# Kernel tuning notes

Hardware: AMD Instinct MI355X
Metric: run time of the kernel (lower is better)

## Reference

```python
import jax, jax.numpy as jnp
import numpy as np

BEAM = 4
START = 1


def setup_inputs() -> dict:
    key = jax.random.key(0)
    ks = jax.random.split(key, 10)
    S, B, H, E, V = 32, 16, 1024, 256, 32000
    Din = E + E + H  # embed + enc_input_step + enc_output_step
    sc = 0.02
    return {
        "enc_h_n": jax.random.normal(ks[0], (1, B, H), jnp.float32),
        "enc_c_n": jax.random.normal(ks[1], (1, B, H), jnp.float32),
        "enc_outputs": jax.random.normal(ks[2], (S, B, H), jnp.float32),
        "enc_inputs": jax.random.normal(ks[3], (S, B, E), jnp.float32),
        "embed": jax.random.normal(ks[4], (V, E), jnp.float32) * sc,
        "w_ih": jax.random.normal(ks[5], (Din, 4 * H), jnp.float32) * sc,
        "w_hh": jax.random.normal(ks[6], (H, 4 * H), jnp.float32) * sc,
        "b_lstm": jnp.zeros((4 * H,), jnp.float32),
        "w_out": jax.random.normal(ks[7], (H, V), jnp.float32) * sc,
        "b_out": jnp.zeros((V,), jnp.float32),
    }


def reference(enc_h_n, enc_c_n, enc_outputs, enc_inputs,
              embed, w_ih, w_hh, b_lstm, w_out, b_out):
    S, B, _ = enc_inputs.shape
    H = enc_h_n.shape[2]
    V = w_out.shape[1]
    K = BEAM

    def decode(word, h, c, ein, eout):
        # word: [B] int, h/c: [B,H], ein: [B,E], eout: [B,H]
        x = jnp.concatenate([embed[word], ein, eout], axis=-1)  # [B,Din]
        gates = x @ w_ih + h @ w_hh + b_lstm                    # [B,4H]
        i, f, g, o = jnp.split(gates, 4, axis=-1)
        c2 = jax.nn.sigmoid(f) * c + jax.nn.sigmoid(i) * jnp.tanh(g)
        h2 = jax.nn.sigmoid(o) * jnp.tanh(c2)
        logits = h2 @ w_out + b_out                             # [B,V]
        return logits, h2, c2

    # ---- init_beam_search (step 0) ----
    h0, c0 = enc_h_n[0], enc_c_n[0]
    word0 = jnp.full((B,), START, dtype=jnp.int32)
    logits0, h1, c1 = decode(word0, h0, c0, enc_inputs[0], enc_outputs[0])
    probs0 = jax.nn.softmax(logits0, axis=-1)
    top_v, top_i = jax.lax.top_k(probs0, K)  # [B,K]
    # NOTE: original code never updates current_scores inside the loop -> constant
    scores = top_v

    h = jnp.broadcast_to(h1, (K, B, H)) + 0.0  # per-beam hidden state copies
    c = jnp.broadcast_to(c1, (K, B, H)) + 0.0
    word = top_i  # [B,K]

    decode_beams = jax.vmap(decode, in_axes=(1, 0, 0, None, None))

    def step(carry, xs):
        h, c, word = carry
        ein, eout = xs
        logits, h2, c2 = decode_beams(word, h, c, ein, eout)  # [K,B,V]
        probs = jax.nn.softmax(logits, axis=-1)
        # space_search layout: beam b occupies cols [b*V, (b+1)*V); tile repeats
        # each beam score V times -> equivalent to broadcast over vocab axis.
        space = jnp.transpose(probs, (1, 0, 2)) * scores[:, :, None]  # [B,K,V]
        _, ti = jax.lax.top_k(space.reshape(B, K * V), K)             # [B,K]
        word2 = ti % V
        return (h2, c2, word2), ti

    (_, _, _), tis = jax.lax.scan(step, (h, c, word),
                                  (enc_inputs[1:], enc_outputs[1:]))
    out = jnp.concatenate([top_i[None], tis], axis=0)  # [S,B,K]
    return jnp.transpose(out, (2, 1, 0)).astype(jnp.int32)  # [K,B,S]
```

## Files before the change

kernel.cpp:

```cpp
#include <hip/hip_runtime.h>
#include <math.h>

#define S_LEN 32
#define B_N   16
#define H_N   1024
#define E_N   256
#define V_N   32000
#define KBEAM 4
#define DIN   1536
#define D2    2560
#define R_N   64
#define NDS   20
#define NB    500

typedef _Float16 f16;
typedef f16   f16x8 __attribute__((ext_vector_type(8)));
typedef float f32x4 __attribute__((ext_vector_type(4)));
#define MFMA(A,B,C) __builtin_amdgcn_mfma_f32_16x16x32_f16(A,B,C,0,0,0)

__device__ __forceinline__ float sigmf(float x){ return 1.0f/(1.0f+expf(-x)); }
__device__ __forceinline__ bool better(float v1,int i1,float v2,int i2){
  return (v1>v2) || (v1==v2 && i1<i2);
}
__device__ __forceinline__ void ins4(float bv,int bi,
    float&av0,float&av1,float&av2,float&av3,int&ai0,int&ai1,int&ai2,int&ai3){
  if (better(bv,bi,av3,ai3)){ av3=bv; ai3=bi;
    if (better(av3,ai3,av2,ai2)){ float t=av2;av2=av3;av3=t; int q=ai2;ai2=ai3;ai3=q;
      if (better(av2,ai2,av1,ai1)){ t=av1;av1=av2;av2=t; q=ai1;ai1=ai2;ai2=q;
        if (better(av1,ai1,av0,ai0)){ t=av0;av0=av1;av1=t; q=ai0;ai0=ai1;ai1=q; } } } }
}

#define FMA16(w4, h4) { \
  acc[0][0]=fmaf(w4.x,h4.x,acc[0][0]); acc[0][1]=fmaf(w4.x,h4.y,acc[0][1]); \
  acc[0][2]=fmaf(w4.x,h4.z,acc[0][2]); acc[0][3]=fmaf(w4.x,h4.w,acc[0][3]); \
  acc[1][0]=fmaf(w4.y,h4.x,acc[1][0]); acc[1][1]=fmaf(w4.y,h4.y,acc[1][1]); \
  acc[1][2]=fmaf(w4.y,h4.z,acc[1][2]); acc[1][3]=fmaf(w4.y,h4.w,acc[1][3]); \
  acc[2][0]=fmaf(w4.z,h4.x,acc[2][0]); acc[2][1]=fmaf(w4.z,h4.y,acc[2][1]); \
  acc[2][2]=fmaf(w4.z,h4.z,acc[2][2]); acc[2][3]=fmaf(w4.z,h4.w,acc[2][3]); \
  acc[3][0]=fmaf(w4.w,h4.x,acc[3][0]); acc[3][1]=fmaf(w4.w,h4.y,acc[3][1]); \
  acc[3][2]=fmaf(w4.w,h4.z,acc[3][2]); acc[3][3]=fmaf(w4.w,h4.w,acc[3][3]); }

__global__ __launch_bounds__(256) void k_init(
    const float* __restrict__ enc_h_n, const float* __restrict__ enc_c_n,
    const float* __restrict__ enc_outputs, const float* __restrict__ enc_inputs,
    const float* __restrict__ embed, float* __restrict__ x, float* __restrict__ c){
  int r = blockIdx.x, tid = threadIdx.x, b = r & 15;
  float* xr = x + (size_t)r*D2;
  xr[tid]        = embed[E_N + tid];
  xr[E_N + tid]  = enc_inputs[b*E_N + tid];
  #pragma unroll
  for (int q=0;q<4;++q) xr[2*E_N + q*256 + tid] = enc_outputs[b*H_N + q*256 + tid];
  #pragma unroll
  for (int q=0;q<4;++q) xr[DIN + q*256 + tid]   = enc_h_n[b*H_N + q*256 + tid];
  #pragma unroll
  for (int q=0;q<4;++q) c[(size_t)r*H_N + q*256 + tid] = enc_c_n[b*H_N + q*256 + tid];
}

__global__ __launch_bounds__(256) void k_convw(
    const float* __restrict__ w, f16* __restrict__ wpk){
  __shared__ f16 Th[64][66];
  __shared__ f16 Tl[64][66];
  int v0 = blockIdx.x*64, d0 = blockIdx.y*64;
  int tid = threadIdx.x;
  int r = tid >> 4, cq = (tid & 15)*4;
  #pragma unroll
  for (int rr=0; rr<4; ++rr){
    int d = r + rr*16;
    float4 x = *(const float4*)&w[(size_t)(d0+d)*V_N + v0 + cq];
    f16 h;
    h=(f16)x.x; Th[d][cq+0]=h; Tl[d][cq+0]=(f16)((x.x-(float)h)*4096.0f);
    h=(f16)x.y; Th[d][cq+1]=h; Tl[d][cq+1]=(f16)((x.y-(float)h)*4096.0f);
    h=(f16)x.z; Th[d][cq+2]=h; Tl[d][cq+2]=(f16)((x.z-(float)h)*4096.0f);
    h=(f16)x.w; Th[d][cq+3]=h; Tl[d][cq+3]=(f16)((x.w-(float)h)*4096.0f);
  }
  __syncthreads();
  int T2 = tid >> 6, l = tid & 63;
  int lm = l & 15, kq = l >> 4;
  int Tg = blockIdx.x*4 + T2;
  #pragma unroll
  for (int ks2=0; ks2<2; ++ks2){
    int ksg = blockIdx.y*2 + ks2;
    f16x8 a, b2;
    #pragma unroll
    for (int i=0;i<8;++i){
      int dd = ks2*32 + kq*8 + i;
      a[i]  = Th[dd][T2*16 + lm];
      b2[i] = Tl[dd][T2*16 + lm];
    }
    size_t base = ((size_t)(Tg*32 + ksg)*2)*512 + l*8;
    *(f16x8*)&wpk[base]       = a;
    *(f16x8*)&wpk[base + 512] = b2;
  }
}

#define GWLD(d, off) (*(const float4*)((((d) < DIN) ? (w_ih + (size_t)(d)*4096) \
                       : (w_hh + (size_t)((d)-DIN)*4096)) + (off)))
__global__ __launch_bounds__(256) void k_gates(
    const float* __restrict__ x, const float* __restrict__ w_ih,
    const float* __restrict__ w_hh, float* __restrict__ gpart){
  int tid = threadIdx.x;
  int jt = blockIdx.x, ks = blockIdx.y;
  int cx = tid & 15, ry = tid >> 4;
  int cb = jt*64;
  int wdd = tid >> 4, wseg = tid & 15;
  int xrow = tid >> 3, xseg = tid & 7;

  __shared__ float Wt0[32][64], Wt1[32][64];
  __shared__ float Xt0[32][68], Xt1[32][68];

  float acc[4][4];
  #pragma unroll
  for (int cc=0;cc<4;++cc)
    #pragma unroll
    for (int rr=0;rr<4;++rr) acc[cc][rr]=0.f;

  int d0 = ks*128;
  const float* xp0 = x + (size_t)xrow*D2 + d0 + xseg*4;
  const float* xp1 = x + (size_t)(xrow+32)*D2 + d0 + xseg*4;

#define GLQ(WA,WB,X0,X1, ch) { int d_ = d0 + (ch)*32; \
  WA = GWLD(d_+wdd,    cb+wseg*4); \
  WB = GWLD(d_+16+wdd, cb+wseg*4); \
  X0 = *(const float4*)(xp0 + (ch)*32); \
  X1 = *(const float4*)(xp1 + (ch)*32); }
#define GSQ(Wt,Xt, WA,WB,X0,X1) { \
  *(float4*)&Wt[wdd][wseg*4]    = WA; \
  *(float4*)&Wt[wdd+16][wseg*4] = WB; \
  Xt[xseg*4+0][xrow] = X0.x; Xt[xseg*4+1][xrow] = X0.y; \
  Xt[xseg*4+2][xrow] = X0.z; Xt[xseg*4+3][xrow] = X0.w; \
  Xt[xseg*4+0][xrow+32] = X1.x; Xt[xseg*4+1][xrow+32] = X1.y; \
  Xt[xseg*4+2][xrow+32] = X1.z; Xt[xseg*4+3][xrow+32] = X1.w; }
#define GCQ(Wt,Xt) { _Pragma("unroll 8") for (int dd=0; dd<32; ++dd){ \
    float4 w4 = *(const float4*)&Wt[dd][cx*4]; \
    float4 h4 = *(const float4*)&Xt[dd][ry*4]; \
    FMA16(w4, h4) } }

  float4 wA0,wB0,x00,x10, wA1,wB1,x01,x11;
  GLQ(wA0,wB0,x00,x10, 0)
  GSQ(Wt0,Xt0, wA0,wB0,x00,x10)
  GLQ(wA1,wB1,x01,x11, 1)
  __syncthreads();

  for (int ch=0; ch<4; ch+=2){
    if (ch+2<4) GLQ(wA0,wB0,x00,x10, ch+2)
    GSQ(Wt1,Xt1, wA1,wB1,x01,x11)
    GCQ(Wt0,Xt0)
    __syncthreads();
    if (ch+3<4) GLQ(wA1,wB1,x01,x11, ch+3)
    if (ch+2<4) GSQ(Wt0,Xt0, wA0,wB0,x00,x10)
    GCQ(Wt1,Xt1)
    if (ch+2<4) __syncthreads();
  }
  #pragma unroll
  for (int rr=0;rr<4;++rr){
    float4 o; o.x=acc[0][rr]; o.y=acc[1][rr]; o.z=acc[2][rr]; o.w=acc[3][rr];
    *(float4*)&gpart[((size_t)(ks*R_N + ry*4+rr))*4096 + cb + cx*4] = o;
  }
}

__global__ __launch_bounds__(256) void k_lstm(
    const float* __restrict__ gpart, const float* __restrict__ b_lstm,
    float* __restrict__ c, float* __restrict__ xn, float* __restrict__ h2t,
    f16* __restrict__ hpk){
  int r = blockIdx.x, tid = threadIdx.x;
  int j = blockIdx.y*256 + tid;
  float gi = b_lstm[j], gf = b_lstm[1024+j], gg = b_lstm[2048+j], go = b_lstm[3072+j];
  #pragma unroll
  for (int ds=0; ds<NDS; ++ds){
    size_t base = ((size_t)ds*R_N + r)*4096;
    gi += gpart[base + j];      gf += gpart[base + 1024 + j];
    gg += gpart[base + 2048+j]; go += gpart[base + 3072 + j];
  }
  float cv = c[(size_t)r*H_N + j];
  float c2 = sigmf(gf)*cv + sigmf(gi)*tanhf(gg);
  float h2 = sigmf(go)*tanhf(c2);
  c[(size_t)r*H_N + j] = c2;
  xn[(size_t)r*D2 + DIN + j] = h2;
  h2t[(size_t)j*R_N + r] = h2;
  f16 hh = (f16)h2;
  int m = r >> 4, lm = r & 15;
  int ks = j >> 5, kq = (j & 31) >> 3, i = j & 7;
  int l = lm + 16*kq;
  size_t base2 = ((size_t)(m*32 + ks)*2)*512 + l*8 + i;
  hpk[base2]       = hh;
  hpk[base2 + 512] = (f16)((h2 - (float)hh)*4096.0f);
}

__global__ __launch_bounds__(256) void k_logits_mfma(
    const f16* __restrict__ wpk, const f16* __restrict__ hpk,
    const float* __restrict__ b_out,
    float* __restrict__ pm, float* __restrict__ pz,
    float* __restrict__ pv, int* __restrict__ pi){
  int tid = threadIdx.x;
  int lane = tid & 63;
  int wv = tid >> 6;
  int T  = blockIdx.x*4 + wv;
  int vb = T*16;

  const f16* wp  = wpk + ((size_t)(T*32))*2*512 + lane*8;
  const f16* hp0 = hpk + ((size_t)(0*32))*2*512 + lane*8;
  const f16* hp1 = hpk + ((size_t)(1*32))*2*512 + lane*8;
  const f16* hp2 = hpk + ((size_t)(2*32))*2*512 + lane*8;
  const f16* hp3 = hpk + ((size_t)(3*32))*2*512 + lane*8;

  f32x4 c10={0,0,0,0}, c11={0,0,0,0}, c12={0,0,0,0}, c13={0,0,0,0};
  f32x4 c20={0,0,0,0}, c21={0,0,0,0}, c22={0,0,0,0}, c23={0,0,0,0};

  f16x8 Bh0,Bl0,A0h0,A1h0,A2h0,A3h0,A0l0,A1l0,A2l0,A3l0;
  f16x8 Bh1,Bl1,A0h1,A1h1,A2h1,A3h1,A0l1,A1l1,A2l1,A3l1;

#define LOADSET(S, s) { size_t o_ = (size_t)(s)*1024; \
  Bh##S  = *(const f16x8*)(wp + o_);  Bl##S  = *(const f16x8*)(wp + o_ + 512); \
  A0h##S = *(const f16x8*)(hp0 + o_); A0l##S = *(const f16x8*)(hp0 + o_ + 512); \
  A1h##S = *(const f16x8*)(hp1 + o_); A1l##S = *(const f16x8*)(hp1 + o_ + 512); \
  A2h##S = *(const f16x8*)(hp2 + o_); A2l##S = *(const f16x8*)(hp2 + o_ + 512); \
  A3h##S = *(const f16x8*)(hp3 + o_); A3l##S = *(const f16x8*)(hp3 + o_ + 512); }
#define COMPSET(S) { \
  c10 = MFMA(A0h##S, Bh##S, c10); c20 = MFMA(A0l##S, Bh##S, c20); c20 = MFMA(A0h##S, Bl##S, c20); \
  c11 = MFMA(A1h##S, Bh##S, c11); c21 = MFMA(A1l##S, Bh##S, c21); c21 = MFMA(A1h##S, Bl##S, c21); \
  c12 = MFMA(A2h##S, Bh##S, c12); c22 = MFMA(A2l##S, Bh##S, c22); c22 = MFMA(A2h##S, Bl##S, c22); \
  c13 = MFMA(A3h##S, Bh##S, c13); c23 = MFMA(A3l##S, Bh##S, c23); c23 = MFMA(A3h##S, Bl##S, c23); }

  LOADSET(0, 0)
  for (int s=0; s<32; s+=2){
    LOADSET(1, s+1)
    COMPSET(0)
    if (s+2<32) LOADSET(0, s+2)
    COMPSET(1)
  }

  __shared__ float Ls[64][68];

  const float inv = 1.0f/4096.0f;
  int lm = lane & 15;
  int rb = (lane>>4)*4;
  float bias = b_out[vb + lm];
#define STT(mt, A1, A2) { \
  _Pragma("unroll") for (int rg=0; rg<4; ++rg){ \
    Ls[(mt)*16 + rb + rg][wv*16 + lm] = A1[rg] + A2[rg]*inv + bias; } }
  STT(0, c10, c20) STT(1, c11, c21) STT(2, c12, c22) STT(3, c13, c23)
  __syncthreads();

  int cx = tid & 15, ry = tid >> 4;
  int cb = blockIdx.x * 64;
  #pragma unroll
  for (int rr=0;rr<4;++rr){
    int row = ry*4 + rr;
    float v0 = Ls[row][cx*4+0], v1 = Ls[row][cx*4+1];
    float v2 = Ls[row][cx*4+2], v3 = Ls[row][cx*4+3];
    int   c0i = cb + cx*4;
    float tv0=-INFINITY,tv1=-INFINITY,tv2=-INFINITY,tv3=-INFINITY;
    int   ti0=0x7fffffff,ti1=0x7fffffff,ti2=0x7fffffff,ti3=0x7fffffff;
    ins4(v0,c0i+0,tv0,tv1,tv2,tv3,ti0,ti1,ti2,ti3);
    ins4(v1,c0i+1,tv0,tv1,tv2,tv3,ti0,ti1,ti2,ti3);
    ins4(v2,c0i+2,tv0,tv1,tv2,tv3,ti0,ti1,ti2,ti3);
    ins4(v3,c0i+3,tv0,tv1,tv2,tv3,ti0,ti1,ti2,ti3);
    float z = expf(v0-tv0)+expf(v1-tv0)+expf(v2-tv0)+expf(v3-tv0);
    #pragma unroll
    for (int msk=1; msk<16; msk<<=1){
      float om  = __shfl_xor(tv0, msk, 16);
      float oz  = __shfl_xor(z,   msk, 16);
      float ov1 = __shfl_xor(tv1, msk, 16);
      float ov2 = __shfl_xor(tv2, msk, 16);
      float ov3 = __shfl_xor(tv3, msk, 16);
      int   oi0 = __shfl_xor(ti0, msk, 16);
      int   oi1 = __shfl_xor(ti1, msk, 16);
      int   oi2 = __shfl_xor(ti2, msk, 16);
      int   oi3 = __shfl_xor(ti3, msk, 16);
      float M = fmaxf(tv0, om);
      z = z*expf(tv0-M) + oz*expf(om-M);
      ins4(om, oi0, tv0,tv1,tv2,tv3, ti0,ti1,ti2,ti3);
      ins4(ov1,oi1, tv0,tv1,tv2,tv3, ti0,ti1,ti2,ti3);
      ins4(ov2,oi2, tv0,tv1,tv2,tv3, ti0,ti1,ti2,ti3);
      ins4(ov3,oi3, tv0,tv1,tv2,tv3, ti0,ti1,ti2,ti3);
    }
    if (cx == 0){
      size_t base = (size_t)row*NB + blockIdx.x;
      pm[base]=tv0; pz[base]=z;
      pv[base*4+0]=tv0; pv[base*4+1]=tv1; pv[base*4+2]=tv2; pv[base*4+3]=tv3;
      pi[base*4+0]=ti0; pi[base*4+1]=ti1; pi[base*4+2]=ti2; pi[base*4+3]=ti3;
    }
  }
}

__global__ __launch_bounds__(256) void k_logits_fused(
    const float* __restrict__ h2t, const float* __restrict__ w_out,
    const float* __restrict__ b_out,
    float* __restrict__ pm, float* __restrict__ pz,
    float* __restrict__ pv, int* __restrict__ pi){
  int tid = threadIdx.x;
  int cx  = tid & 15, ry = tid >> 4;
  int cb  = blockIdx.x * 64;
  int sdd = tid >> 4, seg = tid & 15;
  __shared__ float Wt[32][64];
  __shared__ float Ht[32][64];
  float acc[4][4];
  #pragma unroll
  for (int cc=0;cc<4;++cc)
    #pragma unroll
    for (int rr=0;rr<4;++rr) acc[cc][rr]=0.f;
  const float* gW = w_out + (size_t)sdd*V_N + cb + seg*4;
  const float* gH = h2t + sdd*64 + seg*4;
#define FLQ(WA,WB,HA,HB, ch) { \
  const float* gWn = gW + (size_t)(ch)*32*V_N; \
  const float* gHn = gH + (size_t)(ch)*32*64; \
  WA = *(const float4*)gWn; WB = *(const float4*)(gWn + (size_t)16*V_N); \
  HA = *(const float4*)gHn; HB = *(const float4*)(gHn + 16*64); }
#define FSQ(WA,WB,HA,HB) { \
  *(float4*)&Wt[sdd][seg*4]    = WA; \
  *(float4*)&Wt[sdd+16][seg*4] = WB; \
  *(float4*)&Ht[sdd][seg*4]    = HA; \
  *(float4*)&Ht[sdd+16][seg*4] = HB; }
#define FCQ() { _Pragma("unroll 8") for (int dd=0; dd<32; ++dd){ \
    float4 w4 = *(const float4*)&Wt[dd][cx*4]; \
    float4 h4 = *(const float4*)&Ht[dd][ry*4]; \
    FMA16(w4, h4) } }
  float4 wA0,wB0,hA0,hB0, wA1,wB1,hA1,hB1;
  FLQ(wA0,wB0,hA0,hB0, 0)
  FSQ(wA0,wB0,hA0,hB0)
  FLQ(wA1,wB1,hA1,hB1, 1)
  __syncthreads();
  for (int ch=0; ch<32; ch+=2){
    if (ch+2<32) FLQ(wA0,wB0,hA0,hB0, ch+2)
    FCQ()
    __syncthreads();
    FSQ(wA1,wB1,hA1,hB1)
    __syncthreads();
    if (ch+3<32) FLQ(wA1,wB1,hA1,hB1, ch+3)
    FCQ()
    if (ch+2<32){
      __syncthreads();
      FSQ(wA0,wB0,hA0,hB0)
      __syncthreads();
    }
  }
  float4 bias = *(const float4*)&b_out[cb + cx*4];
  #pragma unroll
  for (int rr=0;rr<4;++rr){
    float v0 = acc[0][rr]+bias.x, v1 = acc[1][rr]+bias.y;
    float v2 = acc[2][rr]+bias.z, v3 = acc[3][rr]+bias.w;
    int   c0i = cb + cx*4;
    float tv0=-INFINITY,tv1=-INFINITY,tv2=-INFINITY,tv3=-INFINITY;
    int   ti0=0x7fffffff,ti1=0x7fffffff,ti2=0x7fffffff,ti3=0x7fffffff;
    ins4(v0,c0i+0,tv0,tv1,tv2,tv3,ti0,ti1,ti2,ti3);
    ins4(v1,c0i+1,tv0,tv1,tv2,tv3,ti0,ti1,ti2,ti3);
    ins4(v2,c0i+2,tv0,tv1,tv2,tv3,ti0,ti1,ti2,ti3);
    ins4(v3,c0i+3,tv0,tv1,tv2,tv3,ti0,ti1,ti2,ti3);
    float z = expf(v0-tv0)+expf(v1-tv0)+expf(v2-tv0)+expf(v3-tv0);
    #pragma unroll
    for (int msk=1; msk<16; msk<<=1){
      float om  = __shfl_xor(tv0, msk, 16);
      float oz  = __shfl_xor(z,   msk, 16);
      float ov1 = __shfl_xor(tv1, msk, 16);
      float ov2 = __shfl_xor(tv2, msk, 16);
      float ov3 = __shfl_xor(tv3, msk, 16);
      int   oi0 = __shfl_xor(ti0, msk, 16);
      int   oi1 = __shfl_xor(ti1, msk, 16);
      int   oi2 = __shfl_xor(ti2, msk, 16);
      int   oi3 = __shfl_xor(ti3, msk, 16);
      float M = fmaxf(tv0, om);
      z = z*expf(tv0-M) + oz*expf(om-M);
      ins4(om, oi0, tv0,tv1,tv2,tv3, ti0,ti1,ti2,ti3);
      ins4(ov1,oi1, tv0,tv1,tv2,tv3, ti0,ti1,ti2,ti3);
      ins4(ov2,oi2, tv0,tv1,tv2,tv3, ti0,ti1,ti2,ti3);
      ins4(ov3,oi3, tv0,tv1,tv2,tv3, ti0,ti1,ti2,ti3);
    }
    if (cx == 0){
      int row = ry*4 + rr;
      size_t base = (size_t)row*NB + blockIdx.x;
      pm[base]=tv0; pz[base]=z;
      pv[base*4+0]=tv0; pv[base*4+1]=tv1; pv[base*4+2]=tv2; pv[base*4+3]=tv3;
      pi[base*4+0]=ti0; pi[base*4+1]=ti1; pi[base*4+2]=ti2; pi[base*4+3]=ti3;
    }
  }
}

__global__ __launch_bounds__(256) void k_final(
    const float* __restrict__ pm, const float* __restrict__ pz,
    const float* __restrict__ pv, const int* __restrict__ pi,
    float* __restrict__ scores, int* __restrict__ out, int t,
    float* __restrict__ xn,
    const float* __restrict__ enc_inputs, const float* __restrict__ enc_outputs,
    const float* __restrict__ embed){
  int b = blockIdx.x, tid = threadIdx.x;
  int kk = tid >> 6, lane = tid & 63;
  __shared__ float fM[KBEAM], fZ[KBEAM], fV[16];
  __shared__ int   fI[16], sw[KBEAM];
  int nk = (t==0) ? 1 : KBEAM;
  if (kk < nk){
    size_t rb = (size_t)(kk*B_N + b)*NB;
    float m=-INFINITY, z=0.f;
    float av0=-INFINITY,av1=-INFINITY,av2=-INFINITY,av3=-INFINITY;
    int   ai0=0x7fffffff,ai1=0x7fffffff,ai2=0x7fffffff,ai3=0x7fffffff;
    for (int p0=lane; p0<NB; p0+=64){
      size_t p = rb + p0;
      float mf = pm[p];
      float M = fmaxf(m, mf);
      z = z*expf(m-M) + pz[p]*expf(mf-M);
      m = M;
      #pragma unroll
      for (int q=0;q<4;++q)
        ins4(pv[p*4+q], pi[p*4+q], av0,av1,av2,av3, ai0,ai1,ai2,ai3);
    }
    #pragma unroll
    for (int msk=1; msk<64; msk<<=1){
      float om  = __shfl_xor(m,   msk);
      float oz  = __shfl_xor(z,   msk);
      float ov0 = __shfl_xor(av0, msk);
      float ov1 = __shfl_xor(av1, msk);
      float ov2 = __shfl_xor(av2, msk);
      float ov3 = __shfl_xor(av3, msk);
      int   oi0 = __shfl_xor(ai0, msk);
      int   oi1 = __shfl_xor(ai1, msk);
      int   oi2 = __shfl_xor(ai2, msk);
      int   oi3 = __shfl_xor(ai3, msk);
      float M = fmaxf(m, om);
      z = z*expf(m-M) + oz*expf(om-M);
      m = M;
      ins4(ov0,oi0, av0,av1,av2,av3, ai0,ai1,ai2,ai3);
      ins4(ov1,oi1, av0,av1,av2,av3, ai0,ai1,ai2,ai3);
      ins4(ov2,oi2, av0,av1,av2,av3, ai0,ai1,ai2,ai3);
      ins4(ov3,oi3, av0,av1,av2,av3, ai0,ai1,ai2,ai3);
    }
    if (lane == 0){
      fM[kk]=m; fZ[kk]=z;
      fV[kk*4+0]=av0; fV[kk*4+1]=av1; fV[kk*4+2]=av2; fV[kk*4+3]=av3;
      fI[kk*4+0]=ai0; fI[kk*4+1]=ai1; fI[kk*4+2]=ai2; fI[kk*4+3]=ai3;
    }
  }
  __syncthreads();
  if (tid==0){
    if (t==0){
      #pragma unroll
      for (int j=0;j<4;++j){
        float p = expf(fV[j]-fM[0])/fZ[0];
        scores[b*4+j] = p;
        out[j*(B_N*S_LEN) + b*S_LEN] = fI[j];
        sw[j] = fI[j];
      }
    } else {
      float cv[16]; int cj[16];
      for (int k=0;k<4;++k){
        float s = scores[b*4+k];
        #pragma unroll
        for (int j=0;j<4;++j){
          cv[k*4+j] = expf(fV[k*4+j]-fM[k])/fZ[k]*s;
          cj[k*4+j] = k*V_N + fI[k*4+j];
        }
      }
      bool used[16];
      for (int i=0;i<16;++i) used[i]=false;
      for (int rank=0;rank<4;++rank){
        int best=-1;
        for (int i=0;i<16;++i){
          if (used[i]) continue;
          if (best<0 || cv[i]>cv[best] || (cv[i]==cv[best] && cj[i]<cj[best])) best=i;
        }
        used[best]=true;
        out[rank*(B_N*S_LEN) + b*S_LEN + t] = cj[best];
        sw[rank] = cj[best] % V_N;
      }
    }
  }
  __syncthreads();
  if (t < S_LEN-1){
    const float* ein = enc_inputs  + (size_t)(t+1)*B_N*E_N + (size_t)b*E_N;
    const float* eo  = enc_outputs + (size_t)(t+1)*B_N*H_N + (size_t)b*H_N;
    #pragma unroll
    for (int j=0;j<KBEAM;++j){
      float* xr = xn + (size_t)(j*B_N + b)*D2;
      const float* em = embed + (size_t)sw[j]*E_N;
      xr[tid]       = em[tid];
      xr[E_N + tid] = ein[tid];
      #pragma unroll
      for (int q=0;q<4;++q) xr[2*E_N + q*256 + tid] = eo[q*256 + tid];
    }
  }
}

extern "C" void kernel_launch(void* const* d_in, const int* in_sizes, int n_in,
                              void* d_out, int out_size, void* d_ws, size_t ws_size,
                              hipStream_t stream) {
  (void)in_sizes; (void)n_in; (void)out_size;
  const float* enc_h_n     = (const float*)d_in[0];
  const float* enc_c_n     = (const float*)d_in[1];
  const float* enc_outputs = (const float*)d_in[2];
  const float* enc_inputs  = (const float*)d_in[3];
  const float* embed       = (const float*)d_in[4];
  const float* w_ih        = (const float*)d_in[5];
  const float* w_hh        = (const float*)d_in[6];
  const float* b_lstm      = (const float*)d_in[7];
  const float* w_out       = (const float*)d_in[8];
  const float* b_out       = (const float*)d_in[9];
  int* out = (int*)d_out;

  float* ws = (float*)d_ws;
  const size_t FRONTF = (size_t)R_N*D2*2 + (size_t)R_N*H_N + (size_t)H_N*R_N;
  const size_t HSPLF  = (size_t)R_N*H_N;
  const size_t GPARTF = (size_t)NDS*R_N*4096;
  const size_t STATF  = (size_t)R_N*NB*10;
  const size_t WSPLF  = (size_t)V_N*H_N;
  size_t need_split = (FRONTF + HSPLF + GPARTF + STATF + 64 + WSPLF)*sizeof(float);
  bool use_split = (ws_size >= need_split);

  float* xA     = ws;
  float* xB     = xA + (size_t)R_N*D2;
  float* cbuf   = xB + (size_t)R_N*D2;
  float* h2t    = cbuf + (size_t)R_N*H_N;
  f16*   hpk    = (f16*)(h2t + (size_t)H_N*R_N);
  float* big    = h2t + (size_t)H_N*R_N + HSPLF;
  float* gpart  = big;
  float* pm     = big + GPARTF;
  float* pz     = pm + (size_t)R_N*NB;
  float* pv     = pz + (size_t)R_N*NB;
  int*   pi     = (int*)(pv + (size_t)R_N*NB*4);
  float* scoresb= (float*)(pi + (size_t)R_N*NB*4);
  f16*   wpk    = (f16*)(scoresb + 64);

  if (use_split){
    k_convw<<<dim3(V_N/64, H_N/64), 256, 0, stream>>>(w_out, wpk);
  }
  k_init<<<R_N, 256, 0, stream>>>(enc_h_n, enc_c_n, enc_outputs, enc_inputs, embed, xA, cbuf);

  for (int t=0; t<S_LEN; ++t){
    float* xc = (t & 1) ? xB : xA;
    float* xn = (t & 1) ? xA : xB;
    k_gates <<<dim3(64, NDS), 256, 0, stream>>>(xc, w_ih, w_hh, gpart);
    k_lstm  <<<dim3(R_N, 4), 256, 0, stream>>>(gpart, b_lstm, cbuf, xn, h2t, hpk);
    if (use_split){
      k_logits_mfma<<<NB, 256, 0, stream>>>(wpk, hpk, b_out, pm, pz, pv, pi);
    } else {
      k_logits_fused<<<NB, 256, 0, stream>>>(h2t, w_out, b_out, pm, pz, pv, pi);
    }
    k_final <<<B_N, 256, 0, stream>>>(pm, pz, pv, pi, scoresb, out, t, xn,
                                      enc_inputs, enc_outputs, embed);
  }
}
```

Before: 2.852 ms.

## Move LSTM gate GEMM to split-fp16 MFMA with pre-packed weights and inputs

```diff
diff --git a/kernel.cpp b/kernel.cpp
--- a/kernel.cpp
+++ b/kernel.cpp
@@ -11,6 +11,7 @@
 #define D2    2560
 #define R_N   64
 #define NDS   20
+#define GKS   4
 #define NB    500
 
 typedef _Float16 f16;
@@ -28,6 +29,16 @@
     if (better(av3,ai3,av2,ai2)){ float t=av2;av2=av3;av3=t; int q=ai2;ai2=ai3;ai3=q;
       if (better(av2,ai2,av1,ai1)){ t=av1;av1=av2;av2=t; q=ai1;ai1=ai2;ai2=q;
         if (better(av1,ai1,av0,ai0)){ t=av0;av0=av1;av1=t; q=ai0;ai0=ai1;ai1=q; } } } }
+}
+
+__device__ __forceinline__ void packx(f16* xpk, int r, int k, float v){
+  int m = r >> 4, lm = r & 15;
+  int ks = k >> 5, kq = (k & 31) >> 3, i = k & 7;
+  int l = lm + 16*kq;
+  size_t base = (((size_t)m*80 + ks)*2)*512 + l*8 + i;
+  f16 hh = (f16)v;
+  xpk[base]       = hh;
+  xpk[base + 512] = (f16)((v - (float)hh)*4096.0f);
 }
 
 #define FMA16(w4, h4) { \
@@ -40,20 +51,52 @@
   acc[3][0]=fmaf(w4.w,h4.x,acc[3][0]); acc[3][1]=fmaf(w4.w,h4.y,acc[3][1]); \
   acc[3][2]=fmaf(w4.w,h4.z,acc[3][2]); acc[3][3]=fmaf(w4.w,h4.w,acc[3][3]); }
 
+#define LOADSET(S, s) { size_t o_ = (size_t)(s)*1024; \
+  Bh##S  = *(const f16x8*)(wp + o_);  Bl##S  = *(const f16x8*)(wp + o_ + 512); \
+  A0h##S = *(const f16x8*)(hp0 + o_); A0l##S = *(const f16x8*)(hp0 + o_ + 512); \
+  A1h##S = *(const f16x8*)(hp1 + o_); A1l##S = *(const f16x8*)(hp1 + o_ + 512); \
+  A2h##S = *(const f16x8*)(hp2 + o_); A2l##S = *(const f16x8*)(hp2 + o_ + 512); \
+  A3h##S = *(const f16x8*)(hp3 + o_); A3l##S = *(const f16x8*)(hp3 + o_ + 512); }
+#define COMPSET(S) { \
+  c10 = MFMA(A0h##S, Bh##S, c10); c20 = MFMA(A0l##S, Bh##S, c20); c20 = MFMA(A0h##S, Bl##S, c20); \
+  c11 = MFMA(A1h##S, Bh##S, c11); c21 = MFMA(A1l##S, Bh##S, c21); c21 = MFMA(A1h##S, Bl##S, c21); \
+  c12 = MFMA(A2h##S, Bh##S, c12); c22 = MFMA(A2l##S, Bh##S, c22); c22 = MFMA(A2h##S, Bl##S, c22); \
+  c13 = MFMA(A3h##S, Bh##S, c13); c23 = MFMA(A3l##S, Bh##S, c23); c23 = MFMA(A3h##S, Bl##S, c23); }
+#define DECLFRAGS \
+  f32x4 c10={0,0,0,0}, c11={0,0,0,0}, c12={0,0,0,0}, c13={0,0,0,0}; \
+  f32x4 c20={0,0,0,0}, c21={0,0,0,0}, c22={0,0,0,0}, c23={0,0,0,0}; \
+  f16x8 Bh0,Bl0,A0h0,A1h0,A2h0,A3h0,A0l0,A1l0,A2l0,A3l0; \
+  f16x8 Bh1,Bl1,A0h1,A1h1,A2h1,A3h1,A0l1,A1l1,A2l1,A3l1;
+
 __global__ __launch_bounds__(256) void k_init(
     const float* __restrict__ enc_h_n, const float* __restrict__ enc_c_n,
     const float* __restrict__ enc_outputs, const float* __restrict__ enc_inputs,
-    const float* __restrict__ embed, float* __restrict__ x, float* __restrict__ c){
+    const float* __restrict__ embed, float* __restrict__ x, float* __restrict__ c,
+    f16* __restrict__ xpk){
   int r = blockIdx.x, tid = threadIdx.x, b = r & 15;
   float* xr = x + (size_t)r*D2;
-  xr[tid]        = embed[E_N + tid];
-  xr[E_N + tid]  = enc_inputs[b*E_N + tid];
-  #pragma unroll
-  for (int q=0;q<4;++q) xr[2*E_N + q*256 + tid] = enc_outputs[b*H_N + q*256 + tid];
-  #pragma unroll
-  for (int q=0;q<4;++q) xr[DIN + q*256 + tid]   = enc_h_n[b*H_N + q*256 + tid];
-  #pragma unroll
-  for (int q=0;q<4;++q) c[(size_t)r*H_N + q*256 + tid] = enc_c_n[b*H_N + q*256 + tid];
+  float v0 = embed[E_N + tid];
+  float v1 = enc_inputs[b*E_N + tid];
+  xr[tid]       = v0;
+  xr[E_N + tid] = v1;
+  float eo[4], hh[4];
+  #pragma unroll
+  for (int q=0;q<4;++q){
+    eo[q] = enc_outputs[b*H_N + q*256 + tid];
+    hh[q] = enc_h_n[b*H_N + q*256 + tid];
+    xr[2*E_N + q*256 + tid] = eo[q];
+    xr[DIN + q*256 + tid]   = hh[q];
+    c[(size_t)r*H_N + q*256 + tid] = enc_c_n[b*H_N + q*256 + tid];
+  }
+  if (xpk){
+    packx(xpk, r, tid, v0);
+    packx(xpk, r, E_N + tid, v1);
+    #pragma unroll
+    for (int q=0;q<4;++q){
+      packx(xpk, r, 2*E_N + q*256 + tid, eo[q]);
+      packx(xpk, r, DIN + q*256 + tid,   hh[q]);
+    }
+  }
 }
 
 __global__ __launch_bounds__(256) void k_convw(
@@ -91,6 +134,83 @@
     *(f16x8*)&wpk[base]       = a;
     *(f16x8*)&wpk[base + 512] = b2;
   }
+}
+
+__global__ __launch_bounds__(256) void k_convg(
+    const float* __restrict__ w_ih, const float* __restrict__ w_hh,
+    f16* __restrict__ wgpk){
+  __shared__ f16 Th[64][66];
+  __shared__ f16 Tl[64][66];
+  int c0 = blockIdx.x*64, k0 = blockIdx.y*64;
+  int tid = threadIdx.x;
+  int r = tid >> 4, cq = (tid & 15)*4;
+  #pragma unroll
+  for (int rr=0; rr<4; ++rr){
+    int d = r + rr*16;
+    int row = k0 + d;
+    const float* src = (row < DIN) ? &w_ih[(size_t)row*4096 + c0 + cq]
+                                   : &w_hh[(size_t)(row-DIN)*4096 + c0 + cq];
+    float4 x = *(const float4*)src;
+    f16 h;
+    h=(f16)x.x; Th[d][cq+0]=h; Tl[d][cq+0]=(f16)((x.x-(float)h)*4096.0f);
+    h=(f16)x.y; Th[d][cq+1]=h; Tl[d][cq+1]=(f16)((x.y-(float)h)*4096.0f);
+    h=(f16)x.z; Th[d][cq+2]=h; Tl[d][cq+2]=(f16)((x.z-(float)h)*4096.0f);
+    h=(f16)x.w; Th[d][cq+3]=h; Tl[d][cq+3]=(f16)((x.w-(float)h)*4096.0f);
+  }
+  __syncthreads();
+  int T2 = tid >> 6, l = tid & 63;
+  int lm = l & 15, kq = l >> 4;
+  int Tg = blockIdx.x*4 + T2;
+  #pragma unroll
+  for (int ks2=0; ks2<2; ++ks2){
+    int ksg = blockIdx.y*2 + ks2;
+    f16x8 a, b2;
+    #pragma unroll
+    for (int i=0;i<8;++i){
+      int dd = ks2*32 + kq*8 + i;
+      a[i]  = Th[dd][T2*16 + lm];
+      b2[i] = Tl[dd][T2*16 + lm];
+    }
+    size_t base = (((size_t)Tg*80 + ksg)*2)*512 + l*8;
+    *(f16x8*)&wgpk[base]       = a;
+    *(f16x8*)&wgpk[base + 512] = b2;
+  }
+}
+
+__global__ __launch_bounds__(256) void k_gates_mfma(
+    const f16* __restrict__ wgpk, const f16* __restrict__ xpk,
+    float* __restrict__ gpart){
+  int tid = threadIdx.x;
+  int lane = tid & 63;
+  int wv = tid >> 6;
+  int T  = blockIdx.x*4 + wv;
+  int ksb = blockIdx.y*20;
+
+  const f16* wp  = wgpk + (((size_t)T*80 + ksb)*2)*512 + lane*8;
+  const f16* hp0 = xpk + (((size_t)0*80 + ksb)*2)*512 + lane*8;
+  const f16* hp1 = xpk + (((size_t)1*80 + ksb)*2)*512 + lane*8;
+  const f16* hp2 = xpk + (((size_t)2*80 + ksb)*2)*512 + lane*8;
+  const f16* hp3 = xpk + (((size_t)3*80 + ksb)*2)*512 + lane*8;
+
+  DECLFRAGS
+
+  LOADSET(0, 0)
+  for (int s=0; s<20; s+=2){
+    LOADSET(1, s+1)
+    COMPSET(0)
+    if (s+2<20) LOADSET(0, s+2)
+    COMPSET(1)
+  }
+
+  const float inv = 1.0f/4096.0f;
+  int lm = lane & 15;
+  int rb = (lane>>4)*4;
+  int col = T*16 + lm;
+  size_t rbase = (size_t)blockIdx.y*R_N;
+#define GSTT(mt, A1, A2) { \
+  _Pragma("unroll") for (int rg=0; rg<4; ++rg){ \
+    gpart[(rbase + (mt)*16 + rb + rg)*4096 + col] = A1[rg] + A2[rg]*inv; } }
+  GSTT(0, c10, c20) GSTT(1, c11, c21) GSTT(2, c12, c22) GSTT(3, c13, c23)
 }
 
 #define GWLD(d, off) (*(const float4*)((((d) < DIN) ? (w_ih + (size_t)(d)*4096) \
@@ -161,12 +281,11 @@
 __global__ __launch_bounds__(256) void k_lstm(
     const float* __restrict__ gpart, const float* __restrict__ b_lstm,
     float* __restrict__ c, float* __restrict__ xn, float* __restrict__ h2t,
-    f16* __restrict__ hpk){
+    f16* __restrict__ hpk, f16* __restrict__ xpk, int nds){
   int r = blockIdx.x, tid = threadIdx.x;
   int j = blockIdx.y*256 + tid;
   float gi = b_lstm[j], gf = b_lstm[1024+j], gg = b_lstm[2048+j], go = b_lstm[3072+j];
-  #pragma unroll
-  for (int ds=0; ds<NDS; ++ds){
+  for (int ds=0; ds<nds; ++ds){
     size_t base = ((size_t)ds*R_N + r)*4096;
     gi += gpart[base + j];      gf += gpart[base + 1024 + j];
     gg += gpart[base + 2048+j]; go += gpart[base + 3072 + j];
@@ -177,13 +296,16 @@
   c[(size_t)r*H_N + j] = c2;
   xn[(size_t)r*D2 + DIN + j] = h2;
   h2t[(size_t)j*R_N + r] = h2;
-  f16 hh = (f16)h2;
-  int m = r >> 4, lm = r & 15;
-  int ks = j >> 5, kq = (j & 31) >> 3, i = j & 7;
-  int l = lm + 16*kq;
-  size_t base2 = ((size_t)(m*32 + ks)*2)*512 + l*8 + i;
-  hpk[base2]       = hh;
-  hpk[base2 + 512] = (f16)((h2 - (float)hh)*4096.0f);
+  if (hpk){
+    f16 hh = (f16)h2;
+    int m = r >> 4, lm = r & 15;
+    int ks = j >> 5, kq = (j & 31) >> 3, i = j & 7;
+    int l = lm + 16*kq;
+    size_t base2 = ((size_t)(m*32 + ks)*2)*512 + l*8 + i;
+    hpk[base2]       = hh;
+    hpk[base2 + 512] = (f16)((h2 - (float)hh)*4096.0f);
+    packx(xpk, r, DIN + j, h2);
+  }
 }
 
 __global__ __launch_bounds__(256) void k_logits_mfma(
@@ -203,23 +325,7 @@
   const f16* hp2 = hpk + ((size_t)(2*32))*2*512 + lane*8;
   const f16* hp3 = hpk + ((size_t)(3*32))*2*512 + lane*8;
 
-  f32x4 c10={0,0,0,0}, c11={0,0,0,0}, c12={0,0,0,0}, c13={0,0,0,0};
-  f32x4 c20={0,0,0,0}, c21={0,0,0,0}, c22={0,0,0,0}, c23={0,0,0,0};
-
-  f16x8 Bh0,Bl0,A0h0,A1h0,A2h0,A3h0,A0l0,A1l0,A2l0,A3l0;
-  f16x8 Bh1,Bl1,A0h1,A1h1,A2h1,A3h1,A0l1,A1l1,A2l1,A3l1;
-
-#define LOADSET(S, s) { size_t o_ = (size_t)(s)*1024; \
-  Bh##S  = *(const f16x8*)(wp + o_);  Bl##S  = *(const f16x8*)(wp + o_ + 512); \
-  A0h##S = *(const f16x8*)(hp0 + o_); A0l##S = *(const f16x8*)(hp0 + o_ + 512); \
-  A1h##S = *(const f16x8*)(hp1 + o_); A1l##S = *(const f16x8*)(hp1 + o_ + 512); \
-  A2h##S = *(const f16x8*)(hp2 + o_); A2l##S = *(const f16x8*)(hp2 + o_ + 512); \
-  A3h##S = *(const f16x8*)(hp3 + o_); A3l##S = *(const f16x8*)(hp3 + o_ + 512); }
-#define COMPSET(S) { \
-  c10 = MFMA(A0h##S, Bh##S, c10); c20 = MFMA(A0l##S, Bh##S, c20); c20 = MFMA(A0h##S, Bl##S, c20); \
-  c11 = MFMA(A1h##S, Bh##S, c11); c21 = MFMA(A1l##S, Bh##S, c21); c21 = MFMA(A1h##S, Bl##S, c21); \
-  c12 = MFMA(A2h##S, Bh##S, c12); c22 = MFMA(A2l##S, Bh##S, c22); c22 = MFMA(A2h##S, Bl##S, c22); \
-  c13 = MFMA(A3h##S, Bh##S, c13); c23 = MFMA(A3l##S, Bh##S, c23); c23 = MFMA(A3h##S, Bl##S, c23); }
+  DECLFRAGS
 
   LOADSET(0, 0)
   for (int s=0; s<32; s+=2){
@@ -379,7 +485,7 @@
     const float* __restrict__ pm, const float* __restrict__ pz,
     const float* __restrict__ pv, const int* __restrict__ pi,
     float* __restrict__ scores, int* __restrict__ out, int t,
-    float* __restrict__ xn,
+    float* __restrict__ xn, f16* __restrict__ xpk,
     const float* __restrict__ enc_inputs, const float* __restrict__ enc_outputs,
     const float* __restrict__ embed){
   int b = blockIdx.x, tid = threadIdx.x;
@@ -468,12 +574,19 @@
     const float* eo  = enc_outputs + (size_t)(t+1)*B_N*H_N + (size_t)b*H_N;
     #pragma unroll
     for (int j=0;j<KBEAM;++j){
-      float* xr = xn + (size_t)(j*B_N + b)*D2;
+      int r = j*B_N + b;
+      float* xr = xn + (size_t)r*D2;
       const float* em = embed + (size_t)sw[j]*E_N;
-      xr[tid]       = em[tid];
-      xr[E_N + tid] = ein[tid];
+      float v0 = em[tid], v1 = ein[tid];
+      xr[tid]       = v0;
+      xr[E_N + tid] = v1;
+      if (xpk){ packx(xpk, r, tid, v0); packx(xpk, r, E_N + tid, v1); }
       #pragma unroll
-      for (int q=0;q<4;++q) xr[2*E_N + q*256 + tid] = eo[q*256 + tid];
+      for (int q=0;q<4;++q){
+        float v = eo[q*256 + tid];
+        xr[2*E_N + q*256 + tid] = v;
+        if (xpk) packx(xpk, r, 2*E_N + q*256 + tid, v);
+      }
     }
   }
 }
@@ -497,10 +610,12 @@
   float* ws = (float*)d_ws;
   const size_t FRONTF = (size_t)R_N*D2*2 + (size_t)R_N*H_N + (size_t)H_N*R_N;
   const size_t HSPLF  = (size_t)R_N*H_N;
+  const size_t XPKF   = (size_t)R_N*D2;
   const size_t GPARTF = (size_t)NDS*R_N*4096;
   const size_t STATF  = (size_t)R_N*NB*10;
   const size_t WSPLF  = (size_t)V_N*H_N;
-  size_t need_split = (FRONTF + HSPLF + GPARTF + STATF + 64 + WSPLF)*sizeof(float);
+  const size_t WGPKF  = (size_t)D2*4096;
+  size_t need_split = (FRONTF + HSPLF + XPKF + GPARTF + STATF + 64 + WSPLF + WGPKF)*sizeof(float);
   bool use_split = (ws_size >= need_split);
 
   float* xA     = ws;
@@ -508,7 +623,8 @@
   float* cbuf   = xB + (size_t)R_N*D2;
   float* h2t    = cbuf + (size_t)R_N*H_N;
   f16*   hpk    = (f16*)(h2t + (size_t)H_N*R_N);
-  float* big    = h2t + (size_t)H_N*R_N + HSPLF;
+  f16*   xpk    = (f16*)(h2t + (size_t)H_N*R_N + HSPLF);
+  float* big    = h2t + (size_t)H_N*R_N + HSPLF + XPKF;
   float* gpart  = big;
   float* pm     = big + GPARTF;
   float* pz     = pm + (size_t)R_N*NB;
@@ -516,23 +632,33 @@
   int*   pi     = (int*)(pv + (size_t)R_N*NB*4);
   float* scoresb= (float*)(pi + (size_t)R_N*NB*4);
   f16*   wpk    = (f16*)(scoresb + 64);
+  f16*   wgpk   = (f16*)((float*)(scoresb + 64) + WSPLF);
+
+  f16* hpk_arg = use_split ? hpk : (f16*)0;
+  f16* xpk_arg = use_split ? xpk : (f16*)0;
 
   if (use_split){
     k_convw<<<dim3(V_N/64, H_N/64), 256, 0, stream>>>(w_out, wpk);
-  }
-  k_init<<<R_N, 256, 0, stream>>>(enc_h_n, enc_c_n, enc_outputs, enc_inputs, embed, xA, cbuf);
+    k_convg<<<dim3(4096/64, D2/64), 256, 0, stream>>>(w_ih, w_hh, wgpk);
+  }
+  k_init<<<R_N, 256, 0, stream>>>(enc_h_n, enc_c_n, enc_outputs, enc_inputs,
+                                  embed, xA, cbuf, xpk_arg);
 
   for (int t=0; t<S_LEN; ++t){
     float* xc = (t & 1) ? xB : xA;
     float* xn = (t & 1) ? xA : xB;
-    k_gates <<<dim3(64, NDS), 256, 0, stream>>>(xc, w_ih, w_hh, gpart);
-    k_lstm  <<<dim3(R_N, 4), 256, 0, stream>>>(gpart, b_lstm, cbuf, xn, h2t, hpk);
     if (use_split){
+      k_gates_mfma<<<dim3(64, GKS), 256, 0, stream>>>(wgpk, xpk, gpart);
+      k_lstm<<<dim3(R_N, 4), 256, 0, stream>>>(gpart, b_lstm, cbuf, xn, h2t,
+                                               hpk_arg, xpk_arg, GKS);
       k_logits_mfma<<<NB, 256, 0, stream>>>(wpk, hpk, b_out, pm, pz, pv, pi);
     } else {
+      k_gates <<<dim3(64, NDS), 256, 0, stream>>>(xc, w_ih, w_hh, gpart);
+      k_lstm<<<dim3(R_N, 4), 256, 0, stream>>>(gpart, b_lstm, cbuf, xn, h2t,
+                                               (f16*)0, (f16*)0, NDS);
       k_logits_fused<<<NB, 256, 0, stream>>>(h2t, w_out, b_out, pm, pz, pv, pi);
     }
-    k_final <<<B_N, 256, 0, stream>>>(pm, pz, pv, pi, scoresb, out, t, xn,
+    k_final <<<B_N, 256, 0, stream>>>(pm, pz, pv, pi, scoresb, out, t, xn, xpk_arg,
                                       enc_inputs, enc_outputs, embed);
   }
 }
```

Result: faster. 2.777 ms (-2.6%).
